# Performance work log

Hardware: AMD Instinct MI355X
Metric: run time of the kernel (lower is better)

## Reference

```python
import jax, jax.numpy as jnp
import numpy as np

D_MODEL = 1024
NUM_HEADS = 16
HEAD_DIM = D_MODEL // NUM_HEADS


def setup_inputs() -> dict:
    key = jax.random.key(0)
    ks = jax.random.split(key, 11)
    B, S, D = 2, 2048, D_MODEL
    scale = 1.0 / np.sqrt(D)
    inp = {
        "query": jax.random.normal(ks[0], (B, S, D), jnp.float32),
        "key": jax.random.normal(ks[1], (B, S, D), jnp.float32),
        "value": jax.random.normal(ks[2], (B, S, D), jnp.float32),
        "Wq": jax.random.normal(ks[3], (D, D), jnp.float32) * scale,
        "bq": jnp.zeros((D,), jnp.float32),
        "Wk": jax.random.normal(ks[4], (D, D), jnp.float32) * scale,
        "bk": jnp.zeros((D,), jnp.float32),
        "Wv": jax.random.normal(ks[5], (D, D), jnp.float32) * scale,
        "bv": jnp.zeros((D,), jnp.float32),
        "Wo": jax.random.normal(ks[6], (D, D), jnp.float32) * scale,
        "bo": jnp.zeros((D,), jnp.float32),
    }
    return inp


def reference(query, key, value, Wq, bq, Wk, bk, Wv, bv, Wo, bo):
    B, S, D = query.shape
    H, hd = NUM_HEADS, HEAD_DIM
    # linear projections (x @ W^T + b, torch nn.Linear convention)
    Q = query @ Wq.T + bq
    K = key @ Wk.T + bk
    V = value @ Wv.T + bv
    # split heads: [B, S, H, hd] -> [B, H, S, hd]
    Q = Q.reshape(B, S, H, hd).transpose(0, 2, 1, 3)
    K = K.reshape(B, S, H, hd).transpose(0, 2, 1, 3)
    V = V.reshape(B, S, H, hd).transpose(0, 2, 1, 3)
    # scaled dot-product attention (explicit, non-flash)
    scores = jnp.einsum("bhqd,bhkd->bhqk", Q, K) / jnp.sqrt(jnp.float32(hd)).astype(Q.dtype)
    attn = jax.nn.softmax(scores, axis=-1)
    out = jnp.einsum("bhqk,bhkd->bhqd", attn, V)
    # merge heads: [B, H, S, hd] -> [B, S, D]
    out = out.transpose(0, 2, 1, 3).reshape(B, S, D)
    return out @ Wo.T + bo
```

## Files before the change

kernel.cpp:

```cpp
#include <hip/hip_runtime.h>
#include <hip/hip_bf16.h>


constexpr int D_MODEL = 1024;
constexpr int S_LEN   = 2048;
constexpr int BATCH   = 2;
constexpr int NH      = 16;
constexpr int HD      = 64;
constexpr int ROWS    = BATCH * S_LEN;

typedef __attribute__((ext_vector_type(8))) short short8;
typedef __attribute__((ext_vector_type(4))) float float4a;

static __device__ __forceinline__ unsigned short f2bf(float f) {
  union { float f; unsigned u; } v{f};
  unsigned r = v.u + 0x7FFFu + ((v.u >> 16) & 1u);
  return (unsigned short)(r >> 16);
}

static __device__ __forceinline__ unsigned pack_bf16(float a, float b) {
#if __has_builtin(__builtin_amdgcn_cvt_pk_bf16_f32)
  typedef __attribute__((ext_vector_type(2))) __bf16 bf16x2;
  union { bf16x2 v; unsigned u; } c;
  c.v = __builtin_amdgcn_cvt_pk_bf16_f32(a, b);
  return c.u;
#else
  return (unsigned)f2bf(a) | ((unsigned)f2bf(b) << 16);
#endif
}

static __device__ __forceinline__ float bf2f(unsigned short u) {
  union { unsigned u; float f; } v;
  v.u = (unsigned)u << 16;
  return v.f;
}

static __device__ __forceinline__ void async16(const void* g, void* l) {
  __builtin_amdgcn_global_load_lds(
      (const __attribute__((address_space(1))) unsigned int*)g,
      (__attribute__((address_space(3))) unsigned int*)l, 16, 0, 0);
}

struct ConvArgs { const float* s[7]; unsigned short* d[7]; int n[7]; };

__global__ __launch_bounds__(256) void convert_bf16(ConvArgs a) {
  const int which = blockIdx.y;
  const int i = (blockIdx.x * 256 + threadIdx.x) * 8;
  if (i >= a.n[which]) return;
  const float4* s = (const float4*)(a.s[which] + i);
  float4 x = s[0], y = s[1];
  unsigned t[4] = {pack_bf16(x.x, x.y), pack_bf16(x.z, x.w),
                   pack_bf16(y.x, y.y), pack_bf16(y.z, y.w)};
  *(short8*)(a.d[which] + i) = *(short8*)t;
}

template <int MODE, int BM>
static __device__ __forceinline__ void gemm_body(
    const unsigned short* __restrict__ A, const unsigned short* __restrict__ W,
    const float* __restrict__ bias, void* __restrict__ Yv, float scale,
    unsigned short* As, unsigned short* Bs, unsigned short* Tb) {
  constexpr int NT = (BM == 128) ? 4 : 2;
  const int tid = threadIdx.x;
  const int w = tid >> 6, lane = tid & 63;
  const int l15 = lane & 15, quad = lane >> 4;
  const int row0 = blockIdx.x * BM, col0 = blockIdx.y * 128;
  const int wm = (BM == 128) ? (w & 1) * 64 : 0;
  const int wn = (BM == 128) ? (w >> 1) * 64 : w * 32;

  float4a acc[4][NT];
#pragma unroll
  for (int i = 0; i < 4; i++)
#pragma unroll
    for (int j = 0; j < NT; j++) acc[i][j] = (float4a){0.f, 0.f, 0.f, 0.f};

  const int swA = (quad + (wm >> 1) + (l15 >> 1)) & 3;
  const int swB = (quad + (wn >> 1) + (l15 >> 1)) & 3;

  for (int kt = 0; kt < D_MODEL; kt += 32) {
    __syncthreads();
#pragma unroll
    for (int j = 0; j < 2; j++) {
      const int i = w * 2 + j;
      const int r = i * 16 + (lane >> 2);
      const int c = ((lane & 3) - (r >> 1)) & 3;
      async16(W + (size_t)(col0 + r) * D_MODEL + kt + c * 8, (char*)Bs + i * 1024);
    }
    if constexpr (BM == 128) {
#pragma unroll
      for (int j = 0; j < 2; j++) {
        const int i = w * 2 + j;
        const int r = i * 16 + (lane >> 2);
        const int c = ((lane & 3) - (r >> 1)) & 3;
        async16(A + (size_t)(row0 + r) * D_MODEL + kt + c * 8, (char*)As + i * 1024);
      }
    } else {
      const int r = w * 16 + (lane >> 2);
      const int c = ((lane & 3) - (r >> 1)) & 3;
      async16(A + (size_t)(row0 + r) * D_MODEL + kt + c * 8, (char*)As + w * 1024);
    }
    __syncthreads();

    short8 af[4], bf[NT];
#pragma unroll
    for (int mt = 0; mt < 4; mt++) {
      const int r = wm + mt * 16 + l15;
      af[mt] = *(const short8*)&As[(r * 4 + swA) * 8];
    }
#pragma unroll
    for (int nt = 0; nt < NT; nt++) {
      const int r = wn + nt * 16 + l15;
      bf[nt] = *(const short8*)&Bs[(r * 4 + swB) * 8];
    }
#pragma unroll
    for (int mt = 0; mt < 4; mt++)
#pragma unroll
      for (int nt = 0; nt < NT; nt++)
        acc[mt][nt] = __builtin_amdgcn_mfma_f32_16x16x32_bf16(af[mt], bf[nt], acc[mt][nt], 0, 0, 0);
  }

  int cols[NT];
  float bvs[NT];
#pragma unroll
  for (int nt = 0; nt < NT; nt++) {
    cols[nt] = col0 + wn + nt * 16 + l15;
    bvs[nt]  = bias[cols[nt]] * ((MODE == 0) ? scale : 1.0f);
  }

  if constexpr (MODE == 0) {
    unsigned short* Y = (unsigned short*)Yv;
#pragma unroll
    for (int mt = 0; mt < 4; mt++)
#pragma unroll
      for (int r = 0; r < 4; r++) {
        const int m = row0 + wm + mt * 16 + quad * 4 + r;
        const int bb = m >> 11, s = m & 2047;
#pragma unroll
        for (int nt = 0; nt < NT; nt++) {
          const int h = cols[nt] >> 6, d = cols[nt] & 63;
          Y[(((size_t)(bb * NH + h)) * S_LEN + s) * HD + d] =
              f2bf(acc[mt][nt][r] * scale + bvs[nt]);
        }
      }
  } else if constexpr (MODE == 2) {
    unsigned short* T = Tb + w * 64 * 64;
#pragma unroll
    for (int mt = 0; mt < 4; mt++)
#pragma unroll
      for (int r = 0; r < 4; r++) {
        const int sl = mt * 16 + quad * 4 + r;
        const int cch = sl >> 3;
#pragma unroll
        for (int nt = 0; nt < NT; nt++) {
          const int dl = cols[nt] - col0 - wn;
          const int slot = cch ^ (dl & 7);
          T[dl * 64 + slot * 8 + (sl & 7)] = f2bf(acc[mt][nt][r] + bvs[nt]);
        }
      }
    asm volatile("s_waitcnt lgkmcnt(0)" ::: "memory");
    unsigned short* Y = (unsigned short*)Yv;
#pragma unroll
    for (int j = 0; j < 8; j++) {
      const int cid = j * 64 + lane;
      const int dl = cid >> 3;
      const int c  = cid & 7;
      const int slot = c ^ (dl & 7);
      short8 v = *(const short8*)&T[dl * 64 + slot * 8];
      const int col = col0 + wn + dl;
      const int h = col >> 6, d = col & 63;
      const int m = row0 + wm + c * 8;
      const int bb = m >> 11, s = m & 2047;
      *(short8*)&Y[(((size_t)(bb * NH + h)) * HD + d) * S_LEN + s] = v;
    }
  } else {
    float* Y = (float*)Yv;
#pragma unroll
    for (int mt = 0; mt < 4; mt++)
#pragma unroll
      for (int r = 0; r < 4; r++) {
        const int m = row0 + wm + mt * 16 + quad * 4 + r;
#pragma unroll
        for (int nt = 0; nt < NT; nt++)
          Y[(size_t)m * D_MODEL + cols[nt]] = acc[mt][nt][r] + bvs[nt];
      }
  }
}

__global__ __launch_bounds__(256) void gemm_qkv(
    const unsigned short* xq, const unsigned short* xk, const unsigned short* xv,
    const unsigned short* wq, const unsigned short* wk, const unsigned short* wv,
    const float* bq, const float* bk, const float* bv,
    unsigned short* Q, unsigned short* K, unsigned short* Vt) {
  __shared__ unsigned short As[128 * 32];
  __shared__ unsigned short Bs[128 * 32];
  __shared__ unsigned short Tb[4 * 64 * 64];
  const int z = blockIdx.z;
  if (z == 0)      gemm_body<0, 128>(xq, wq, bq, Q,  0.125f * 1.44269504f, As, Bs, Tb);
  else if (z == 1) gemm_body<0, 128>(xk, wk, bk, K,  1.0f,   As, Bs, Tb);
  else             gemm_body<2, 128>(xv, wv, bv, Vt, 1.0f,   As, Bs, Tb);
}

__global__ __launch_bounds__(256) void gemm_o(const unsigned short* o16, const unsigned short* wo,
                                              const float* bo, float* out) {
  __shared__ unsigned short As[64 * 32];
  __shared__ unsigned short Bs[128 * 32];
  gemm_body<3, 64>(o16, wo, bo, out, 1.0f, As, Bs, nullptr);
}

__global__ __launch_bounds__(256) void attn_kernel(
    const unsigned short* __restrict__ Qh, const unsigned short* __restrict__ Kh,
    const unsigned short* __restrict__ Vt, unsigned short* __restrict__ Op,
    float* __restrict__ Lp) {
  const int qb = blockIdx.x;
  const int h  = blockIdx.y;
  const int bb = blockIdx.z >> 1, sp = blockIdx.z & 1;
  const int tid = threadIdx.x;
  const int w = tid >> 6, lane = tid & 63;
  const int l15 = lane & 15, quad = lane >> 4;

  __shared__ unsigned short Ks[64 * 64];
  __shared__ unsigned short Vs[64 * 64];
  __shared__ unsigned short Ps[4][32][72];

  const size_t bh = (size_t)(bb * NH + h);
  const unsigned short* Qp = Qh + bh * S_LEN * HD;
  const unsigned short* Kp = Kh + bh * S_LEN * HD;
  const unsigned short* Vp = Vt + bh * (size_t)HD * S_LEN;

  short8 qf[2][2];
#pragma unroll
  for (int qnt = 0; qnt < 2; qnt++)
#pragma unroll
    for (int c = 0; c < 2; c++)
      qf[qnt][c] = *(const short8*)(Qp + (size_t)(qb * 128 + w * 32 + qnt * 16 + l15) * HD +
                                    c * 32 + quad * 8);

  unsigned short ob[8] = {0x3F80, 0x3F80, 0x3F80, 0x3F80, 0x3F80, 0x3F80, 0x3F80, 0x3F80};
  const short8 ones = *(short8*)ob;

  float4a Oacc[2][4];
#pragma unroll
  for (int a = 0; a < 2; a++)
#pragma unroll
    for (int b = 0; b < 4; b++) Oacc[a][b] = (float4a){0.f, 0.f, 0.f, 0.f};
  float4a Lacc[2] = {(float4a){0.f, 0.f, 0.f, 0.f}, (float4a){0.f, 0.f, 0.f, 0.f}};

  const int sw0 = (quad + l15) & 7;
  const int sw1 = (quad + 4 + l15) & 7;

  for (int kb = sp * 1024; kb < sp * 1024 + 1024; kb += 64) {
    __syncthreads();
#pragma unroll
    for (int j = 0; j < 2; j++) {
      const int i = w * 2 + j;
      const int r = i * 8 + (lane >> 3);
      const int c = ((lane & 7) - r) & 7;
      async16(Kp + (size_t)(kb + r) * HD + c * 8, (char*)Ks + i * 1024);
      async16(Vp + (size_t)r * S_LEN + kb + c * 8, (char*)Vs + i * 1024);
    }
    __syncthreads();

#pragma unroll
    for (int mt = 0; mt < 4; mt++) {
      const int rb = (mt * 16 + l15) * 8;
      short8 a0 = *(const short8*)&Ks[(rb + sw0) * 8];
      short8 a1 = *(const short8*)&Ks[(rb + sw1) * 8];
#pragma unroll
      for (int qnt = 0; qnt < 2; qnt++) {
        float4a s = (float4a){0.f, 0.f, 0.f, 0.f};
        s = __builtin_amdgcn_mfma_f32_16x16x32_bf16(a0, qf[qnt][0], s, 0, 0, 0);
        s = __builtin_amdgcn_mfma_f32_16x16x32_bf16(a1, qf[qnt][1], s, 0, 0, 0);
        uint2 pk;
        pk.x = pack_bf16(__builtin_amdgcn_exp2f(s[0]), __builtin_amdgcn_exp2f(s[1]));
        pk.y = pack_bf16(__builtin_amdgcn_exp2f(s[2]), __builtin_amdgcn_exp2f(s[3]));
        *(uint2*)&Ps[w][qnt * 16 + l15][mt * 16 + quad * 4] = pk;
      }
    }
    asm volatile("s_waitcnt lgkmcnt(0)" ::: "memory");

#pragma unroll
    for (int c = 0; c < 2; c++) {
      short8 pa0 = *(const short8*)&Ps[w][l15][c * 32 + quad * 8];
      short8 pa1 = *(const short8*)&Ps[w][16 + l15][c * 32 + quad * 8];
      Lacc[0] = __builtin_amdgcn_mfma_f32_16x16x32_bf16(pa0, ones, Lacc[0], 0, 0, 0);
      Lacc[1] = __builtin_amdgcn_mfma_f32_16x16x32_bf16(pa1, ones, Lacc[1], 0, 0, 0);
      const int vsw = (c * 4 + quad + l15) & 7;
#pragma unroll
      for (int nt = 0; nt < 4; nt++) {
        short8 vb = *(const short8*)&Vs[((nt * 16 + l15) * 8 + vsw) * 8];
        Oacc[0][nt] = __builtin_amdgcn_mfma_f32_16x16x32_bf16(pa0, vb, Oacc[0][nt], 0, 0, 0);
        Oacc[1][nt] = __builtin_amdgcn_mfma_f32_16x16x32_bf16(pa1, vb, Oacc[1][nt], 0, 0, 0);
      }
    }
  }

  if (l15 == 0) {
#pragma unroll
    for (int qnt = 0; qnt < 2; qnt++)
#pragma unroll
      for (int reg = 0; reg < 4; reg++) {
        const int q = qb * 128 + w * 32 + qnt * 16 + quad * 4 + reg;
        Lp[(size_t)sp * ROWS * NH + ((size_t)bb * S_LEN + q) * NH + h] = Lacc[qnt][reg];
      }
  }

  unsigned short* Ob = Op + (size_t)sp * ROWS * D_MODEL;
#pragma unroll
  for (int qnt = 0; qnt < 2; qnt++) {
#pragma unroll
    for (int reg = 0; reg < 4; reg++) {
      const int q = qb * 128 + w * 32 + qnt * 16 + quad * 4 + reg;
      unsigned short* orow = Ob + ((size_t)bb * S_LEN + q) * D_MODEL + h * HD;
#pragma unroll
      for (int nt = 0; nt < 4; nt++)
        orow[nt * 16 + l15] = f2bf(Oacc[qnt][nt][reg]);
    }
  }
}

__global__ __launch_bounds__(256) void merge_kernel(const unsigned short* __restrict__ Op,
                                                    const float* __restrict__ Lp,
                                                    unsigned short* __restrict__ obuf) {
  const int e = (blockIdx.x * 256 + threadIdx.x) * 8;
  const int row = e >> 10, h = (e & 1023) >> 6;
  const float l = Lp[(size_t)row * NH + h] + Lp[(size_t)ROWS * NH + (size_t)row * NH + h];
  const float rinv = 1.0f / l;
  short8 a = *(const short8*)(Op + e);
  short8 b = *(const short8*)(Op + (size_t)ROWS * D_MODEL + e);
  unsigned t[4];
#pragma unroll
  for (int i = 0; i < 4; i++) {
    const float v0 = (bf2f((unsigned short)a[2 * i]) + bf2f((unsigned short)b[2 * i])) * rinv;
    const float v1 = (bf2f((unsigned short)a[2 * i + 1]) + bf2f((unsigned short)b[2 * i + 1])) * rinv;
    t[i] = pack_bf16(v0, v1);
  }
  *(short8*)(obuf + e) = *(short8*)t;
}

extern "C" void kernel_launch(void* const* d_in, const int* in_sizes, int n_in,
                              void* d_out, int out_size, void* d_ws, size_t ws_size,
                              hipStream_t stream) {
  const float* query = (const float*)d_in[0];
  const float* key   = (const float*)d_in[1];
  const float* value = (const float*)d_in[2];
  const float* Wq = (const float*)d_in[3];
  const float* bq = (const float*)d_in[4];
  const float* Wk = (const float*)d_in[5];
  const float* bk = (const float*)d_in[6];
  const float* Wv = (const float*)d_in[7];
  const float* bv = (const float*)d_in[8];
  const float* Wo = (const float*)d_in[9];
  const float* bo = (const float*)d_in[10];
  float* out = (float*)d_out;

  char* ws = (char*)d_ws;
  const size_t MB = 1024 * 1024;
  unsigned short* xq16 = (unsigned short*)(ws + 0 * MB);
  unsigned short* xk16 = (unsigned short*)(ws + 8 * MB);
  unsigned short* xv16 = (unsigned short*)(ws + 16 * MB);
  unsigned short* wq16 = (unsigned short*)(ws + 24 * MB);
  unsigned short* wk16 = (unsigned short*)(ws + 26 * MB);
  unsigned short* wv16 = (unsigned short*)(ws + 28 * MB);
  unsigned short* qbuf  = (unsigned short*)(ws + 32 * MB);
  unsigned short* kbuf  = (unsigned short*)(ws + 40 * MB);
  unsigned short* vtbuf = (unsigned short*)(ws + 48 * MB);
  unsigned short* wo16  = (unsigned short*)(ws + 56 * MB);
  float* Lp  = (float*)(ws + 58 * MB);
  unsigned short* Op = (unsigned short*)(ws + 0 * MB);
  unsigned short* obuf = qbuf;

  ConvArgs ca;
  const int NX = ROWS * D_MODEL, NW = D_MODEL * D_MODEL;
  ca.s[0] = query; ca.d[0] = xq16; ca.n[0] = NX;
  ca.s[1] = key;   ca.d[1] = xk16; ca.n[1] = NX;
  ca.s[2] = value; ca.d[2] = xv16; ca.n[2] = NX;
  ca.s[3] = Wq;    ca.d[3] = wq16; ca.n[3] = NW;
  ca.s[4] = Wk;    ca.d[4] = wk16; ca.n[4] = NW;
  ca.s[5] = Wv;    ca.d[5] = wv16; ca.n[5] = NW;
  ca.s[6] = Wo;    ca.d[6] = wo16; ca.n[6] = NW;
  hipLaunchKernelGGL(convert_bf16, dim3(NX / 2048, 7), dim3(256), 0, stream, ca);

  dim3 gqkv(ROWS / 128, D_MODEL / 128, 3);
  hipLaunchKernelGGL(gemm_qkv, gqkv, dim3(256), 0, stream,
                     xq16, xk16, xv16, wq16, wk16, wv16, bq, bk, bv,
                     qbuf, kbuf, vtbuf);

  dim3 ga(S_LEN / 128, NH, BATCH * 2);
  hipLaunchKernelGGL(attn_kernel, ga, dim3(256), 0, stream, qbuf, kbuf, vtbuf, Op, Lp);

  hipLaunchKernelGGL(merge_kernel, dim3(ROWS * D_MODEL / 2048), dim3(256), 0, stream,
                     Op, Lp, obuf);

  dim3 go(ROWS / 64, D_MODEL / 128);
  hipLaunchKernelGGL(gemm_o, go, dim3(256), 0, stream, obuf, wo16, bo, out);
}
```

Before: 236.1 us.

## Double-buffer LDS tiles in GEMM and attention loops to overlap loads

Adds ping-pong shared-memory buffers to the projection GEMMs and the attention K/V loop. The async global-to-LDS copy for the next tile is issued before computing on the current one, and one barrier per iteration replaces two. The aim is to hide global load latency behind MFMA work. In exchange, LDS use per block grows, which could lower occupancy, and the V-output transpose buffer now aliases the GEMM staging memory, so an extra barrier guards it.

```diff
diff --git a/kernel.cpp b/kernel.cpp
--- a/kernel.cpp
+++ b/kernel.cpp
@@ -54,12 +54,41 @@
   *(short8*)(a.d[which] + i) = *(short8*)t;
 }
 
+template <int BM>
+static __device__ __forceinline__ void gemm_stage(
+    const unsigned short* A, const unsigned short* W, int row0, int col0,
+    int w, int lane, unsigned short* As, unsigned short* Bs, int kt, int par) {
+  unsigned short* Bd = Bs + par * (128 * 32);
+#pragma unroll
+  for (int j = 0; j < 2; j++) {
+    const int i = w * 2 + j;
+    const int r = i * 16 + (lane >> 2);
+    const int c = ((lane & 3) - (r >> 1)) & 3;
+    async16(W + (size_t)(col0 + r) * D_MODEL + kt + c * 8, (char*)Bd + i * 1024);
+  }
+  unsigned short* Ad = As + par * (BM * 32);
+  if constexpr (BM == 128) {
+#pragma unroll
+    for (int j = 0; j < 2; j++) {
+      const int i = w * 2 + j;
+      const int r = i * 16 + (lane >> 2);
+      const int c = ((lane & 3) - (r >> 1)) & 3;
+      async16(A + (size_t)(row0 + r) * D_MODEL + kt + c * 8, (char*)Ad + i * 1024);
+    }
+  } else {
+    const int r = w * 16 + (lane >> 2);
+    const int c = ((lane & 3) - (r >> 1)) & 3;
+    async16(A + (size_t)(row0 + r) * D_MODEL + kt + c * 8, (char*)Ad + w * 1024);
+  }
+}
+
 template <int MODE, int BM>
 static __device__ __forceinline__ void gemm_body(
     const unsigned short* __restrict__ A, const unsigned short* __restrict__ W,
     const float* __restrict__ bias, void* __restrict__ Yv, float scale,
     unsigned short* As, unsigned short* Bs, unsigned short* Tb) {
   constexpr int NT = (BM == 128) ? 4 : 2;
+  constexpr int KI = D_MODEL / 32;
   const int tid = threadIdx.x;
   const int w = tid >> 6, lane = tid & 63;
   const int l15 = lane & 15, quad = lane >> 4;
@@ -76,40 +105,26 @@
   const int swA = (quad + (wm >> 1) + (l15 >> 1)) & 3;
   const int swB = (quad + (wn >> 1) + (l15 >> 1)) & 3;
 
-  for (int kt = 0; kt < D_MODEL; kt += 32) {
+  gemm_stage<BM>(A, W, row0, col0, w, lane, As, Bs, 0, 0);
+
+  for (int it = 0; it < KI; ++it) {
     __syncthreads();
-#pragma unroll
-    for (int j = 0; j < 2; j++) {
-      const int i = w * 2 + j;
-      const int r = i * 16 + (lane >> 2);
-      const int c = ((lane & 3) - (r >> 1)) & 3;
-      async16(W + (size_t)(col0 + r) * D_MODEL + kt + c * 8, (char*)Bs + i * 1024);
-    }
-    if constexpr (BM == 128) {
-#pragma unroll
-      for (int j = 0; j < 2; j++) {
-        const int i = w * 2 + j;
-        const int r = i * 16 + (lane >> 2);
-        const int c = ((lane & 3) - (r >> 1)) & 3;
-        async16(A + (size_t)(row0 + r) * D_MODEL + kt + c * 8, (char*)As + i * 1024);
-      }
-    } else {
-      const int r = w * 16 + (lane >> 2);
-      const int c = ((lane & 3) - (r >> 1)) & 3;
-      async16(A + (size_t)(row0 + r) * D_MODEL + kt + c * 8, (char*)As + w * 1024);
-    }
-    __syncthreads();
+    if (it + 1 < KI)
+      gemm_stage<BM>(A, W, row0, col0, w, lane, As, Bs, (it + 1) * 32, (it + 1) & 1);
+    const int par = it & 1;
+    const unsigned short* Ab = As + par * (BM * 32);
+    const unsigned short* Bb = Bs + par * (128 * 32);
 
     short8 af[4], bf[NT];
 #pragma unroll
     for (int mt = 0; mt < 4; mt++) {
       const int r = wm + mt * 16 + l15;
-      af[mt] = *(const short8*)&As[(r * 4 + swA) * 8];
+      af[mt] = *(const short8*)&Ab[(r * 4 + swA) * 8];
     }
 #pragma unroll
     for (int nt = 0; nt < NT; nt++) {
       const int r = wn + nt * 16 + l15;
-      bf[nt] = *(const short8*)&Bs[(r * 4 + swB) * 8];
+      bf[nt] = *(const short8*)&Bb[(r * 4 + swB) * 8];
     }
 #pragma unroll
     for (int mt = 0; mt < 4; mt++)
@@ -142,6 +157,7 @@
         }
       }
   } else if constexpr (MODE == 2) {
+    __syncthreads();
     unsigned short* T = Tb + w * 64 * 64;
 #pragma unroll
     for (int mt = 0; mt < 4; mt++)
@@ -190,19 +206,20 @@
     const unsigned short* wq, const unsigned short* wk, const unsigned short* wv,
     const float* bq, const float* bk, const float* bv,
     unsigned short* Q, unsigned short* K, unsigned short* Vt) {
-  __shared__ unsigned short As[128 * 32];
-  __shared__ unsigned short Bs[128 * 32];
-  __shared__ unsigned short Tb[4 * 64 * 64];
+  __shared__ unsigned short smem[4 * 128 * 32];
+  unsigned short* As = smem;
+  unsigned short* Bs = smem + 2 * 128 * 32;
+  unsigned short* Tb = smem;
   const int z = blockIdx.z;
   if (z == 0)      gemm_body<0, 128>(xq, wq, bq, Q,  0.125f * 1.44269504f, As, Bs, Tb);
-  else if (z == 1) gemm_body<0, 128>(xk, wk, bk, K,  1.0f,   As, Bs, Tb);
-  else             gemm_body<2, 128>(xv, wv, bv, Vt, 1.0f,   As, Bs, Tb);
+  else if (z == 1) gemm_body<0, 128>(xk, wk, bk, K,  1.0f, As, Bs, Tb);
+  else             gemm_body<2, 128>(xv, wv, bv, Vt, 1.0f, As, Bs, Tb);
 }
 
 __global__ __launch_bounds__(256) void gemm_o(const unsigned short* o16, const unsigned short* wo,
                                               const float* bo, float* out) {
-  __shared__ unsigned short As[64 * 32];
-  __shared__ unsigned short Bs[128 * 32];
+  __shared__ unsigned short As[2 * 64 * 32];
+  __shared__ unsigned short Bs[2 * 128 * 32];
   gemm_body<3, 64>(o16, wo, bo, out, 1.0f, As, Bs, nullptr);
 }
 
@@ -217,8 +234,8 @@
   const int w = tid >> 6, lane = tid & 63;
   const int l15 = lane & 15, quad = lane >> 4;
 
-  __shared__ unsigned short Ks[64 * 64];
-  __shared__ unsigned short Vs[64 * 64];
+  __shared__ unsigned short Ks[2][64 * 64];
+  __shared__ unsigned short Vs[2][64 * 64];
   __shared__ unsigned short Ps[4][32][72];
 
   const size_t bh = (size_t)(bb * NH + h);
@@ -247,23 +264,30 @@
   const int sw0 = (quad + l15) & 7;
   const int sw1 = (quad + 4 + l15) & 7;
 
-  for (int kb = sp * 1024; kb < sp * 1024 + 1024; kb += 64) {
-    __syncthreads();
+  auto stage = [&](int kb, int par) {
 #pragma unroll
     for (int j = 0; j < 2; j++) {
       const int i = w * 2 + j;
       const int r = i * 8 + (lane >> 3);
       const int c = ((lane & 7) - r) & 7;
-      async16(Kp + (size_t)(kb + r) * HD + c * 8, (char*)Ks + i * 1024);
-      async16(Vp + (size_t)r * S_LEN + kb + c * 8, (char*)Vs + i * 1024);
-    }
+      async16(Kp + (size_t)(kb + r) * HD + c * 8, (char*)&Ks[par][0] + i * 1024);
+      async16(Vp + (size_t)r * S_LEN + kb + c * 8, (char*)&Vs[par][0] + i * 1024);
+    }
+  };
+
+  const int kb0 = sp * 1024;
+  stage(kb0, 0);
+
+  for (int t = 0; t < 16; ++t) {
     __syncthreads();
+    if (t + 1 < 16) stage(kb0 + (t + 1) * 64, (t + 1) & 1);
+    const int par = t & 1;
 
 #pragma unroll
     for (int mt = 0; mt < 4; mt++) {
       const int rb = (mt * 16 + l15) * 8;
-      short8 a0 = *(const short8*)&Ks[(rb + sw0) * 8];
-      short8 a1 = *(const short8*)&Ks[(rb + sw1) * 8];
+      short8 a0 = *(const short8*)&Ks[par][(rb + sw0) * 8];
+      short8 a1 = *(const short8*)&Ks[par][(rb + sw1) * 8];
 #pragma unroll
       for (int qnt = 0; qnt < 2; qnt++) {
         float4a s = (float4a){0.f, 0.f, 0.f, 0.f};
@@ -286,7 +310,7 @@
       const int vsw = (c * 4 + quad + l15) & 7;
 #pragma unroll
       for (int nt = 0; nt < 4; nt++) {
-        short8 vb = *(const short8*)&Vs[((nt * 16 + l15) * 8 + vsw) * 8];
+        short8 vb = *(const short8*)&Vs[par][((nt * 16 + l15) * 8 + vsw) * 8];
         Oacc[0][nt] = __builtin_amdgcn_mfma_f32_16x16x32_bf16(pa0, vb, Oacc[0][nt], 0, 0, 0);
         Oacc[1][nt] = __builtin_amdgcn_mfma_f32_16x16x32_bf16(pa1, vb, Oacc[1][nt], 0, 0, 0);
       }
```

Result: slower. 244.9 us (+3.7%).

## Fuse split-KV merge into output projection GEMM and shrink QKV shared memory

Applied to the files above, without the earlier changes.

Removes the separate merge kernel: the output-projection GEMM now loads both split-KV partial outputs and the softmax denominators, normalizes and packs to bf16 in registers, then stores into the LDS A tile before the MFMA loop. The QKV GEMM now reuses its A/B tile buffers for the V transpose staging, doing the transpose in two halves so shared memory per block drops, which may allow higher occupancy. This trades an intermediate global round trip and a launch for redundant merge work across the column blocks of gemm_o and synchronous (non-async) A-tile loading.

```diff
diff --git a/kernel.cpp b/kernel.cpp
--- a/kernel.cpp
+++ b/kernel.cpp
@@ -54,24 +54,22 @@
   *(short8*)(a.d[which] + i) = *(short8*)t;
 }
 
-template <int MODE, int BM>
+template <int MODE>
 static __device__ __forceinline__ void gemm_body(
     const unsigned short* __restrict__ A, const unsigned short* __restrict__ W,
     const float* __restrict__ bias, void* __restrict__ Yv, float scale,
     unsigned short* As, unsigned short* Bs, unsigned short* Tb) {
-  constexpr int NT = (BM == 128) ? 4 : 2;
   const int tid = threadIdx.x;
   const int w = tid >> 6, lane = tid & 63;
   const int l15 = lane & 15, quad = lane >> 4;
-  const int row0 = blockIdx.x * BM, col0 = blockIdx.y * 128;
-  const int wm = (BM == 128) ? (w & 1) * 64 : 0;
-  const int wn = (BM == 128) ? (w >> 1) * 64 : w * 32;
-
-  float4a acc[4][NT];
+  const int row0 = blockIdx.x * 128, col0 = blockIdx.y * 128;
+  const int wm = (w & 1) * 64, wn = (w >> 1) * 64;
+
+  float4a acc[4][4];
 #pragma unroll
   for (int i = 0; i < 4; i++)
 #pragma unroll
-    for (int j = 0; j < NT; j++) acc[i][j] = (float4a){0.f, 0.f, 0.f, 0.f};
+    for (int j = 0; j < 4; j++) acc[i][j] = (float4a){0.f, 0.f, 0.f, 0.f};
 
   const int swA = (quad + (wm >> 1) + (l15 >> 1)) & 3;
   const int swB = (quad + (wn >> 1) + (l15 >> 1)) & 3;
@@ -84,44 +82,32 @@
       const int r = i * 16 + (lane >> 2);
       const int c = ((lane & 3) - (r >> 1)) & 3;
       async16(W + (size_t)(col0 + r) * D_MODEL + kt + c * 8, (char*)Bs + i * 1024);
-    }
-    if constexpr (BM == 128) {
-#pragma unroll
-      for (int j = 0; j < 2; j++) {
-        const int i = w * 2 + j;
-        const int r = i * 16 + (lane >> 2);
-        const int c = ((lane & 3) - (r >> 1)) & 3;
-        async16(A + (size_t)(row0 + r) * D_MODEL + kt + c * 8, (char*)As + i * 1024);
-      }
-    } else {
-      const int r = w * 16 + (lane >> 2);
-      const int c = ((lane & 3) - (r >> 1)) & 3;
-      async16(A + (size_t)(row0 + r) * D_MODEL + kt + c * 8, (char*)As + w * 1024);
-    }
-    __syncthreads();
-
-    short8 af[4], bf[NT];
+      async16(A + (size_t)(row0 + r) * D_MODEL + kt + c * 8, (char*)As + i * 1024);
+    }
+    __syncthreads();
+
+    short8 af[4], bf[4];
 #pragma unroll
     for (int mt = 0; mt < 4; mt++) {
       const int r = wm + mt * 16 + l15;
       af[mt] = *(const short8*)&As[(r * 4 + swA) * 8];
     }
 #pragma unroll
-    for (int nt = 0; nt < NT; nt++) {
+    for (int nt = 0; nt < 4; nt++) {
       const int r = wn + nt * 16 + l15;
       bf[nt] = *(const short8*)&Bs[(r * 4 + swB) * 8];
     }
 #pragma unroll
     for (int mt = 0; mt < 4; mt++)
 #pragma unroll
-      for (int nt = 0; nt < NT; nt++)
+      for (int nt = 0; nt < 4; nt++)
         acc[mt][nt] = __builtin_amdgcn_mfma_f32_16x16x32_bf16(af[mt], bf[nt], acc[mt][nt], 0, 0, 0);
   }
 
-  int cols[NT];
-  float bvs[NT];
-#pragma unroll
-  for (int nt = 0; nt < NT; nt++) {
+  int cols[4];
+  float bvs[4];
+#pragma unroll
+  for (int nt = 0; nt < 4; nt++) {
     cols[nt] = col0 + wn + nt * 16 + l15;
     bvs[nt]  = bias[cols[nt]] * ((MODE == 0) ? scale : 1.0f);
   }
@@ -135,53 +121,49 @@
         const int m = row0 + wm + mt * 16 + quad * 4 + r;
         const int bb = m >> 11, s = m & 2047;
 #pragma unroll
-        for (int nt = 0; nt < NT; nt++) {
+        for (int nt = 0; nt < 4; nt++) {
           const int h = cols[nt] >> 6, d = cols[nt] & 63;
           Y[(((size_t)(bb * NH + h)) * S_LEN + s) * HD + d] =
               f2bf(acc[mt][nt][r] * scale + bvs[nt]);
         }
       }
-  } else if constexpr (MODE == 2) {
-    unsigned short* T = Tb + w * 64 * 64;
-#pragma unroll
-    for (int mt = 0; mt < 4; mt++)
-#pragma unroll
-      for (int r = 0; r < 4; r++) {
-        const int sl = mt * 16 + quad * 4 + r;
-        const int cch = sl >> 3;
-#pragma unroll
-        for (int nt = 0; nt < NT; nt++) {
-          const int dl = cols[nt] - col0 - wn;
-          const int slot = cch ^ (dl & 7);
-          T[dl * 64 + slot * 8 + (sl & 7)] = f2bf(acc[mt][nt][r] + bvs[nt]);
+  } else {
+    __syncthreads();
+    unsigned short* T = Tb + w * (64 * 32);
+    unsigned short* Y = (unsigned short*)Yv;
+#pragma unroll
+    for (int p = 0; p < 2; p++) {
+      if (p) { asm volatile("s_waitcnt lgkmcnt(0)" ::: "memory"); }
+#pragma unroll
+      for (int mi = 0; mi < 2; mi++) {
+        const int mt = 2 * p + mi;
+#pragma unroll
+        for (int r = 0; r < 4; r++) {
+          const int sl = mi * 16 + quad * 4 + r;
+          const int cch = sl >> 3;
+#pragma unroll
+          for (int nt = 0; nt < 4; nt++) {
+            const int dl = nt * 16 + l15;
+            const int slot = cch ^ (dl & 3);
+            T[dl * 32 + slot * 8 + (sl & 7)] = f2bf(acc[mt][nt][r] + bvs[nt]);
+          }
         }
       }
-    asm volatile("s_waitcnt lgkmcnt(0)" ::: "memory");
-    unsigned short* Y = (unsigned short*)Yv;
-#pragma unroll
-    for (int j = 0; j < 8; j++) {
-      const int cid = j * 64 + lane;
-      const int dl = cid >> 3;
-      const int c  = cid & 7;
-      const int slot = c ^ (dl & 7);
-      short8 v = *(const short8*)&T[dl * 64 + slot * 8];
-      const int col = col0 + wn + dl;
-      const int h = col >> 6, d = col & 63;
-      const int m = row0 + wm + c * 8;
-      const int bb = m >> 11, s = m & 2047;
-      *(short8*)&Y[(((size_t)(bb * NH + h)) * HD + d) * S_LEN + s] = v;
-    }
-  } else {
-    float* Y = (float*)Yv;
-#pragma unroll
-    for (int mt = 0; mt < 4; mt++)
-#pragma unroll
-      for (int r = 0; r < 4; r++) {
-        const int m = row0 + wm + mt * 16 + quad * 4 + r;
-#pragma unroll
-        for (int nt = 0; nt < NT; nt++)
-          Y[(size_t)m * D_MODEL + cols[nt]] = acc[mt][nt][r] + bvs[nt];
-      }
+      asm volatile("s_waitcnt lgkmcnt(0)" ::: "memory");
+#pragma unroll
+      for (int j = 0; j < 4; j++) {
+        const int cid = j * 64 + lane;
+        const int dl = cid >> 2;
+        const int c  = cid & 3;
+        const int slot = c ^ (dl & 3);
+        short8 v = *(const short8*)&T[dl * 32 + slot * 8];
+        const int col = col0 + wn + dl;
+        const int h = col >> 6, d = col & 63;
+        const int m = row0 + wm + p * 32 + c * 8;
+        const int bb = m >> 11, s = m & 2047;
+        *(short8*)&Y[(((size_t)(bb * NH + h)) * HD + d) * S_LEN + s] = v;
+      }
+    }
   }
 }
 
@@ -190,20 +172,99 @@
     const unsigned short* wq, const unsigned short* wk, const unsigned short* wv,
     const float* bq, const float* bk, const float* bv,
     unsigned short* Q, unsigned short* K, unsigned short* Vt) {
-  __shared__ unsigned short As[128 * 32];
-  __shared__ unsigned short Bs[128 * 32];
-  __shared__ unsigned short Tb[4 * 64 * 64];
+  __shared__ unsigned short smem[2 * 128 * 32];
+  unsigned short* As = smem;
+  unsigned short* Bs = smem + 128 * 32;
+  unsigned short* Tb = smem;
   const int z = blockIdx.z;
-  if (z == 0)      gemm_body<0, 128>(xq, wq, bq, Q,  0.125f * 1.44269504f, As, Bs, Tb);
-  else if (z == 1) gemm_body<0, 128>(xk, wk, bk, K,  1.0f,   As, Bs, Tb);
-  else             gemm_body<2, 128>(xv, wv, bv, Vt, 1.0f,   As, Bs, Tb);
-}
-
-__global__ __launch_bounds__(256) void gemm_o(const unsigned short* o16, const unsigned short* wo,
-                                              const float* bo, float* out) {
+  if (z == 0)      gemm_body<0>(xq, wq, bq, Q,  0.125f * 1.44269504f, As, Bs, Tb);
+  else if (z == 1) gemm_body<0>(xk, wk, bk, K,  1.0f, As, Bs, Tb);
+  else             gemm_body<2>(xv, wv, bv, Vt, 1.0f, As, Bs, Tb);
+}
+
+__global__ __launch_bounds__(256) void gemm_o(
+    const unsigned short* __restrict__ Op, const float* __restrict__ Lp,
+    const unsigned short* __restrict__ wo, const float* __restrict__ bo,
+    float* __restrict__ out) {
   __shared__ unsigned short As[64 * 32];
   __shared__ unsigned short Bs[128 * 32];
-  gemm_body<3, 64>(o16, wo, bo, out, 1.0f, As, Bs, nullptr);
+  const int tid = threadIdx.x;
+  const int w = tid >> 6, lane = tid & 63;
+  const int l15 = lane & 15, quad = lane >> 4;
+  const int row0 = blockIdx.x * 64, col0 = blockIdx.y * 128;
+  const int wn = w * 32;
+
+  const int ar = w * 16 + (lane >> 2);
+  const int cg = lane & 3;
+  const int asl = (cg + (ar >> 1)) & 3;
+  const int grow = row0 + ar;
+  const unsigned short* P0 = Op + (size_t)grow * D_MODEL + cg * 8;
+  const unsigned short* P1 = P0 + (size_t)ROWS * D_MODEL;
+  const float* L0 = Lp + (size_t)grow * NH;
+  const float* L1 = L0 + (size_t)ROWS * NH;
+
+  float4a acc[4][2];
+#pragma unroll
+  for (int i = 0; i < 4; i++)
+#pragma unroll
+    for (int j = 0; j < 2; j++) acc[i][j] = (float4a){0.f, 0.f, 0.f, 0.f};
+
+  const int swA = (quad + (l15 >> 1)) & 3;
+  const int swB = (quad + (wn >> 1) + (l15 >> 1)) & 3;
+
+  for (int kt = 0; kt < D_MODEL; kt += 32) {
+    const int h = kt >> 6;
+    const float rinv = 1.0f / (L0[h] + L1[h]);
+    short8 a = *(const short8*)(P0 + kt);
+    short8 b = *(const short8*)(P1 + kt);
+    unsigned t[4];
+#pragma unroll
+    for (int i = 0; i < 4; i++) {
+      const float v0 = (bf2f((unsigned short)a[2 * i]) + bf2f((unsigned short)b[2 * i])) * rinv;
+      const float v1 = (bf2f((unsigned short)a[2 * i + 1]) + bf2f((unsigned short)b[2 * i + 1])) * rinv;
+      t[i] = pack_bf16(v0, v1);
+    }
+    __syncthreads();
+    *(short8*)&As[(ar * 4 + asl) * 8] = *(short8*)t;
+#pragma unroll
+    for (int j = 0; j < 2; j++) {
+      const int i = w * 2 + j;
+      const int r = i * 16 + (lane >> 2);
+      const int c = ((lane & 3) - (r >> 1)) & 3;
+      async16(wo + (size_t)(col0 + r) * D_MODEL + kt + c * 8, (char*)Bs + i * 1024);
+    }
+    __syncthreads();
+
+    short8 af[4], bf[2];
+#pragma unroll
+    for (int mt = 0; mt < 4; mt++) {
+      const int r = mt * 16 + l15;
+      af[mt] = *(const short8*)&As[(r * 4 + swA) * 8];
+    }
+#pragma unroll
+    for (int nt = 0; nt < 2; nt++) {
+      const int r = wn + nt * 16 + l15;
+      bf[nt] = *(const short8*)&Bs[(r * 4 + swB) * 8];
+    }
+#pragma unroll
+    for (int mt = 0; mt < 4; mt++)
+#pragma unroll
+      for (int nt = 0; nt < 2; nt++)
+        acc[mt][nt] = __builtin_amdgcn_mfma_f32_16x16x32_bf16(af[mt], bf[nt], acc[mt][nt], 0, 0, 0);
+  }
+
+#pragma unroll
+  for (int nt = 0; nt < 2; nt++) {
+    const int col = col0 + wn + nt * 16 + l15;
+    const float bv = bo[col];
+#pragma unroll
+    for (int mt = 0; mt < 4; mt++)
+#pragma unroll
+      for (int r = 0; r < 4; r++) {
+        const int m = row0 + mt * 16 + quad * 4 + r;
+        out[(size_t)m * D_MODEL + col] = acc[mt][nt][r] + bv;
+      }
+  }
 }
 
 __global__ __launch_bounds__(256) void attn_kernel(
@@ -315,25 +376,6 @@
         orow[nt * 16 + l15] = f2bf(Oacc[qnt][nt][reg]);
     }
   }
-}
-
-__global__ __launch_bounds__(256) void merge_kernel(const unsigned short* __restrict__ Op,
-                                                    const float* __restrict__ Lp,
-                                                    unsigned short* __restrict__ obuf) {
-  const int e = (blockIdx.x * 256 + threadIdx.x) * 8;
-  const int row = e >> 10, h = (e & 1023) >> 6;
-  const float l = Lp[(size_t)row * NH + h] + Lp[(size_t)ROWS * NH + (size_t)row * NH + h];
-  const float rinv = 1.0f / l;
-  short8 a = *(const short8*)(Op + e);
-  short8 b = *(const short8*)(Op + (size_t)ROWS * D_MODEL + e);
-  unsigned t[4];
-#pragma unroll
-  for (int i = 0; i < 4; i++) {
-    const float v0 = (bf2f((unsigned short)a[2 * i]) + bf2f((unsigned short)b[2 * i])) * rinv;
-    const float v1 = (bf2f((unsigned short)a[2 * i + 1]) + bf2f((unsigned short)b[2 * i + 1])) * rinv;
-    t[i] = pack_bf16(v0, v1);
-  }
-  *(short8*)(obuf + e) = *(short8*)t;
 }
 
 extern "C" void kernel_launch(void* const* d_in, const int* in_sizes, int n_in,
@@ -364,9 +406,8 @@
   unsigned short* kbuf  = (unsigned short*)(ws + 40 * MB);
   unsigned short* vtbuf = (unsigned short*)(ws + 48 * MB);
   unsigned short* wo16  = (unsigned short*)(ws + 56 * MB);
-  float* Lp  = (float*)(ws + 58 * MB);
+  float* Lp = (float*)(ws + 58 * MB);
   unsigned short* Op = (unsigned short*)(ws + 0 * MB);
-  unsigned short* obuf = qbuf;
 
   ConvArgs ca;
   const int NX = ROWS * D_MODEL, NW = D_MODEL * D_MODEL;
@@ -387,9 +428,6 @@
   dim3 ga(S_LEN / 128, NH, BATCH * 2);
   hipLaunchKernelGGL(attn_kernel, ga, dim3(256), 0, stream, qbuf, kbuf, vtbuf, Op, Lp);
 
-  hipLaunchKernelGGL(merge_kernel, dim3(ROWS * D_MODEL / 2048), dim3(256), 0, stream,
-                     Op, Lp, obuf);
-
   dim3 go(ROWS / 64, D_MODEL / 128);
-  hipLaunchKernelGGL(gemm_o, go, dim3(256), 0, stream, obuf, wo16, bo, out);
-}
+  hipLaunchKernelGGL(gemm_o, go, dim3(256), 0, stream, Op, Lp, wo16, bo, out);
+}
```

Result: no change. 232.3 us (-1.6%).
